# Kernel optimization log

Hardware: AMD Instinct MI355X
Metric: run time of the kernel (lower is better)

Reference implementation:

```python
import jax, jax.numpy as jnp
import numpy as np

N = 50000          # num nodes
E = 800000         # num edges (before self loops)
IN_C = 128
HID = 256          # heads * head_dim
HEADS = 4
HEAD_DIM = HID // HEADS
OUT_C = 64
NEG_SLOPE = 0.2    # PyG GATConv default leaky_relu slope
BN_EPS = 1e-5


def _gat_conv(x, src, dst, W, att_src, att_dst, bias, concat):
    """PyG-style GATConv (with self loops already appended to src/dst).
    x: [N, in_c]; W: [in_c, H*C]; att_src/att_dst: [H, C]; bias: [H*C] or [C]."""
    H, C = att_src.shape
    h = (x @ W).reshape(-1, H, C)                               # [N, H, C]
    a_src = jnp.einsum('nhc,hc->nh', h, att_src)                # [N, H]
    a_dst = jnp.einsum('nhc,hc->nh', h, att_dst)                # [N, H]
    e = jax.nn.leaky_relu(a_src[src] + a_dst[dst], NEG_SLOPE)   # [Et, H]
    # segment softmax over destination nodes (numerically stable)
    m = jax.ops.segment_max(e, dst, num_segments=N)             # [N, H]
    m = jnp.where(jnp.isfinite(m), m, 0.0)
    ex = jnp.exp(e - m[dst])
    denom = jax.ops.segment_sum(ex, dst, num_segments=N)        # [N, H]
    alpha = ex / (denom[dst] + 1e-16)                           # [Et, H]
    msg = alpha[:, :, None] * h[src]                            # [Et, H, C]
    out = jax.ops.segment_sum(msg, dst, num_segments=N)         # [N, H, C]
    out = out.reshape(N, H * C) if concat else out.mean(axis=1)
    return out + bias


def _bn_eval(x, gamma, beta, mean, var):
    return (x - mean) * jax.lax.rsqrt(var + BN_EPS) * gamma + beta


def setup_inputs() -> dict:
    key = jax.random.key(0)
    ks = jax.random.split(key, 16)
    x = jax.random.normal(ks[0], (N, IN_C), dtype=jnp.float32)
    edge_index = jax.random.randint(ks[1], (2, E), 0, N, dtype=jnp.int64)

    def lin(k, fan_in, fan_out):
        s = (1.0 / np.sqrt(fan_in)).astype(np.float32)
        return jax.random.normal(k, (fan_in, fan_out), dtype=jnp.float32) * s

    def att(k, h, c):
        return jax.random.normal(k, (h, c), dtype=jnp.float32) * 0.1

    return {
        'x': x, 'edge_index': edge_index,
        'W0': lin(ks[2], IN_C, HID), 'as0': att(ks[3], HEADS, HEAD_DIM), 'ad0': att(ks[4], HEADS, HEAD_DIM), 'b0': jnp.zeros((HID,), jnp.float32),
        'bn0_g': jnp.ones((HID,), jnp.float32), 'bn0_b': jnp.zeros((HID,), jnp.float32), 'bn0_m': jnp.zeros((HID,), jnp.float32), 'bn0_v': jnp.ones((HID,), jnp.float32),
        'W1': lin(ks[5], HID, HID), 'as1': att(ks[6], HEADS, HEAD_DIM), 'ad1': att(ks[7], HEADS, HEAD_DIM), 'b1': jnp.zeros((HID,), jnp.float32),
        'bn1_g': jnp.ones((HID,), jnp.float32), 'bn1_b': jnp.zeros((HID,), jnp.float32), 'bn1_m': jnp.zeros((HID,), jnp.float32), 'bn1_v': jnp.ones((HID,), jnp.float32),
        'W2': lin(ks[8], HID, OUT_C), 'as2': att(ks[9], 1, OUT_C), 'ad2': att(ks[10], 1, OUT_C), 'b2': jnp.zeros((OUT_C,), jnp.float32),
    }


def reference(x, edge_index, W0, as0, ad0, b0, bn0_g, bn0_b, bn0_m, bn0_v,
              W1, as1, ad1, b1, bn1_g, bn1_b, bn1_m, bn1_v,
              W2, as2, ad2, b2):
    loop = jnp.arange(N, dtype=edge_index.dtype)
    src = jnp.concatenate([edge_index[0], loop])   # PyG add_self_loops=True
    dst = jnp.concatenate([edge_index[1], loop])

    h = _gat_conv(x, src, dst, W0, as0, ad0, b0, concat=True)
    h = jax.nn.elu(_bn_eval(h, bn0_g, bn0_b, bn0_m, bn0_v))   # dropout: eval -> identity
    h = _gat_conv(h, src, dst, W1, as1, ad1, b1, concat=True)
    h = jax.nn.elu(_bn_eval(h, bn1_g, bn1_b, bn1_m, bn1_v))
    out = _gat_conv(h, src, dst, W2, as2, ad2, b2, concat=False)  # heads=1, mean
    return out
```

## Files before the change

kernel.cpp:

```cpp
#include <hip/hip_runtime.h>

#define NN   50000
#define EE   800000
#define ET   850000
#define INC  128
#define HID  256
#define OUTC 64
#define NEG  0.2f
#define BNEPS 1e-5f

typedef __bf16 bf16x8 __attribute__((ext_vector_type(8)));
typedef float  f32x4  __attribute__((ext_vector_type(4)));

static __device__ __forceinline__ float b2f(unsigned short u) {
    return __uint_as_float(((unsigned)u) << 16);
}
static __device__ __forceinline__ float blo(unsigned u) {
    return __uint_as_float(u << 16);
}
static __device__ __forceinline__ float bhi(unsigned u) {
    return __uint_as_float(u & 0xFFFF0000u);
}
static __device__ __forceinline__ unsigned short f2b(float f) {
    unsigned u = __float_as_uint(f);
    unsigned r = u + 0x7FFFu + ((u >> 16) & 1u);
    return (unsigned short)(r >> 16);
}
static __device__ __forceinline__ float leaky(float x) {
    return x > 0.f ? x : NEG * x;
}
static __device__ __forceinline__ float ew(float e) {
    return __expf(fminf(e, 80.f));
}

__global__ void k_flags(const int* __restrict__ ei, const unsigned* __restrict__ xw,
                        int* __restrict__ flagW, int* __restrict__ flagB) {
    __shared__ int cs[4];
    int b = blockIdx.x, t = threadIdx.x;
    if (b == 0) {
        int c = 0;
        for (int k = 0; k < 16; k++) {
            int i = t + 256 * k;
            if (ei[2 * i + 1] != 0) c = 1;
        }
        for (int o = 1; o < 64; o <<= 1) c |= __shfl_xor(c, o);
        if ((t & 63) == 0) cs[t >> 6] = c;
        __syncthreads();
        if (t == 0) *flagW = cs[0] | cs[1] | cs[2] | cs[3];
    } else {
        int c = 0;
        for (int i = t; i < 4096; i += 256) {
            unsigned v = (xw[i] >> 8) & 0x7F;
            if (v >= 50 && v <= 67) c++;
        }
        for (int o = 1; o < 64; o <<= 1) c += __shfl_xor(c, o);
        if ((t & 63) == 0) cs[t >> 6] = c;
        __syncthreads();
        if (t == 0) *flagB = (cs[0] + cs[1] + cs[2] + cs[3] > 2048) ? 1 : 0;
    }
}

__global__ void k_prep(const void* as0, const void* ad0, const void* b0, const void* g0,
                       const void* be0, const void* m0, const void* v0,
                       const void* as1, const void* ad1, const void* b1, const void* g1,
                       const void* be1, const void* m1, const void* v1,
                       const void* as2, const void* ad2, const void* b2,
                       const void* W0, const void* W1, const void* W2,
                       unsigned short* __restrict__ WT0, unsigned short* __restrict__ WT1,
                       unsigned short* __restrict__ WT2,
                       const void* __restrict__ x, unsigned short* __restrict__ xb,
                       float* __restrict__ pp, const int* __restrict__ flagB) {
    int b = blockIdx.x, t = threadIdx.x;
    bool bf = (*flagB != 0);
    auto cv = [&](const void* s, int i) -> float {
        return bf ? b2f(((const unsigned short*)s)[i]) : ((const float*)s)[i];
    };
    if (b < 14) {
        float v;
        switch (b) {
            case 0:  v = cv(as0, t); break;
            case 1:  v = cv(ad0, t); break;
            case 2:  v = cv(b0, t);  break;
            case 3:  v = cv(g0, t);  break;
            case 4:  v = cv(be0, t); break;
            case 5:  v = cv(m0, t);  break;
            case 6:  v = cv(v0, t);  break;
            case 7:  v = cv(as1, t); break;
            case 8:  v = cv(ad1, t); break;
            case 9:  v = cv(b1, t);  break;
            case 10: v = cv(g1, t);  break;
            case 11: v = cv(be1, t); break;
            case 12: v = cv(m1, t);  break;
            default: v = cv(v1, t);  break;
        }
        pp[b * 256 + t] = v;
    } else if (b == 14) {
        if (t < 192) {
            int arr = t >> 6, j = t & 63;
            float v = (arr == 0) ? cv(as2, j) : (arr == 1) ? cv(ad2, j) : cv(b2, j);
            pp[14 * 256 + arr * 64 + j] = v;
        }
    } else if (b < 15 + 128) {
        int i = (b - 15) * 256 + t;
        int k = i >> 8, n = i & 255;
        WT0[n * INC + k] = bf ? ((const unsigned short*)W0)[i] : f2b(((const float*)W0)[i]);
    } else if (b < 15 + 128 + 256) {
        int i = (b - 143) * 256 + t;
        int k = i >> 8, n = i & 255;
        WT1[n * HID + k] = bf ? ((const unsigned short*)W1)[i] : f2b(((const float*)W1)[i]);
    } else if (b < 15 + 128 + 256 + 64) {
        int i = (b - 399) * 256 + t;
        int k = i >> 6, n = i & 63;
        WT2[n * HID + k] = bf ? ((const unsigned short*)W2)[i] : f2b(((const float*)W2)[i]);
    } else {
        if (bf) return;
        int i = (b - 463) * 256 + t;
        if (i < NN * INC)
            xb[i] = f2b(((const float*)x)[i]);
    }
}

__global__ void k_hist(const int* __restrict__ ei, const int* __restrict__ flagW,
                       int* __restrict__ cnt) {
    int i = blockIdx.x * 256 + threadIdx.x;
    if (i >= ET) return;
    bool w32 = (*flagW != 0);
    int d = (i < EE) ? (w32 ? ei[EE + i] : ei[2 * (EE + i)]) : (i - EE);
    atomicAdd(&cnt[d], 1);
}

static __device__ __forceinline__ int block_scan_incl(int v, int t, int* ws) {
    int lane = t & 63, w = t >> 6;
    int x = v;
    for (int o = 1; o < 64; o <<= 1) {
        int y = __shfl_up(x, o);
        if (lane >= o) x += y;
    }
    if (lane == 63) ws[w] = x;
    __syncthreads();
    if (t == 0) {
        int s = 0;
        for (int k = 0; k < 4; k++) { int tmp = ws[k]; ws[k] = s; s += tmp; }
    }
    __syncthreads();
    return x + ws[w];
}

__global__ void k_scan_a(const int* __restrict__ cnt, int* __restrict__ rowptr, int* __restrict__ bsum) {
    __shared__ int ws[4];
    int t = threadIdx.x, b = blockIdx.x;
    int i = b * 256 + t;
    int v = (i < NN) ? cnt[i] : 0;
    int incl = block_scan_incl(v, t, ws);
    if (i < NN) rowptr[i] = incl - v;
    if (t == 255) bsum[b] = incl;
}

__global__ void k_scan_b(int* __restrict__ bsum, int nb) {
    __shared__ int ws[4];
    int t = threadIdx.x;
    int v = (t < nb) ? bsum[t] : 0;
    int incl = block_scan_incl(v, t, ws);
    if (t < nb) bsum[t] = incl - v;
}

__global__ void k_scan_c(int* __restrict__ rowptr, const int* __restrict__ bsum, int* __restrict__ cursor) {
    int t = threadIdx.x, b = blockIdx.x;
    int i = b * 256 + t;
    if (i < NN) {
        int r = rowptr[i] + bsum[b];
        rowptr[i] = r;
        cursor[i] = r;
    }
    if (i == 0) rowptr[NN] = ET;
}

__global__ void k_scatter(const int* __restrict__ ei, const int* __restrict__ flagW,
                          int* __restrict__ cursor, int* __restrict__ esrc) {
    int i = blockIdx.x * 256 + threadIdx.x;
    if (i >= ET) return;
    bool w32 = (*flagW != 0);
    int s, d;
    if (i < EE) {
        if (w32) { s = ei[i];     d = ei[EE + i]; }
        else     { s = ei[2 * i]; d = ei[2 * (EE + i)]; }
    } else {
        s = d = i - EE;
    }
    int p = atomicAdd(&cursor[d], 1);
    esrc[p] = s;
}

template<int NC, int NH>
__global__ __launch_bounds__(256) void k_gemm(const unsigned short* __restrict__ Amain,
                                              const void* __restrict__ Aalt,
                                              const int* __restrict__ flagB,
                                              const unsigned short* __restrict__ WT,
                                              unsigned short* __restrict__ H,
                                              float* __restrict__ asrc, float* __restrict__ adst,
                                              const float* __restrict__ asv, const float* __restrict__ adv,
                                              int M, int K) {
    __shared__ __align__(16) unsigned short As[128 * 40];
    __shared__ __align__(16) unsigned short Bs[64 * 40];
    const unsigned short* A = (*flagB) ? (const unsigned short*)Aalt : Amain;
    int t = threadIdx.x;
    int bm = blockIdx.x, bn = blockIdx.y;
    int lane = t & 63, wave = t >> 6;
    int m16 = lane & 15, quad = lane >> 4;

    f32x4 acc[2][4];
    for (int a = 0; a < 2; a++) for (int b = 0; b < 4; b++) acc[a][b] = (f32x4){0.f, 0.f, 0.f, 0.f};

    int arow = t >> 1, ahalf = t & 1;
    int brow = t >> 2, bq = t & 3;
    long gArow = (long)bm * 128 + arow;

    for (int k0 = 0; k0 < K; k0 += 32) {
        uint4 av0 = {0u, 0u, 0u, 0u}, av1 = {0u, 0u, 0u, 0u};
        if (gArow < M) {
            const unsigned short* ap = A + gArow * (size_t)K + k0 + ahalf * 16;
            av0 = *(const uint4*)(ap);
            av1 = *(const uint4*)(ap + 8);
        }
        uint4 bv = *(const uint4*)(WT + ((size_t)bn * 64 + brow) * K + k0 + bq * 8);
        *(uint4*)&As[arow * 40 + ahalf * 16]     = av0;
        *(uint4*)&As[arow * 40 + ahalf * 16 + 8] = av1;
        *(uint4*)&Bs[brow * 40 + bq * 8]         = bv;
        __syncthreads();
        int wrow = wave * 32;
        bf16x8 af[2], bf[4];
        for (int mt = 0; mt < 2; mt++)
            af[mt] = *(const bf16x8*)&As[(wrow + mt * 16 + m16) * 40 + quad * 8];
        for (int nt = 0; nt < 4; nt++)
            bf[nt] = *(const bf16x8*)&Bs[(nt * 16 + m16) * 40 + quad * 8];
        for (int mt = 0; mt < 2; mt++)
            for (int nt = 0; nt < 4; nt++)
                acc[mt][nt] = __builtin_amdgcn_mfma_f32_16x16x32_bf16(af[mt], bf[nt], acc[mt][nt], 0, 0, 0);
        __syncthreads();
    }

    float asc[4], adc[4];
    for (int nt = 0; nt < 4; nt++) {
        int col = bn * 64 + nt * 16 + m16;
        asc[nt] = asv[col];
        adc[nt] = adv[col];
    }
    for (int mt = 0; mt < 2; mt++) {
        int gR0 = bm * 128 + wave * 32 + mt * 16 + quad * 4;
        for (int r = 0; r < 4; r++) {
            int gR = gR0 + r;
            float ps = 0.f, pd = 0.f;
            for (int nt = 0; nt < 4; nt++) {
                float v = acc[mt][nt][r];
                ps += v * asc[nt];
                pd += v * adc[nt];
            }
            for (int o = 1; o < 16; o <<= 1) { ps += __shfl_xor(ps, o); pd += __shfl_xor(pd, o); }
            if (m16 == 0 && gR < M) {
                asrc[(size_t)gR * NH + bn] = ps;
                adst[(size_t)gR * NH + bn] = pd;
            }
            if (gR < M) {
                for (int nt = 0; nt < 4; nt++) {
                    int gC = bn * 64 + nt * 16 + m16;
                    H[(size_t)gR * NC + gC] = f2b(acc[mt][nt][r]);
                }
            }
        }
    }
}

__global__ void k_agg4(const unsigned short* __restrict__ h,
                       const float* __restrict__ asrc, const float* __restrict__ adst,
                       const int* __restrict__ rowptr, const int* __restrict__ esrc,
                       const float* __restrict__ bias,
                       const float* __restrict__ bng, const float* __restrict__ bnb,
                       const float* __restrict__ bnm, const float* __restrict__ bnv,
                       unsigned short* __restrict__ act) {
    int t = threadIdx.x;
    int wave = t >> 6, lane = t & 63;
    int nodeA = blockIdx.x * 8 + wave * 2;
    if (nodeA >= NN) return;
    int nodeB = nodeA + 1;
    bool hasB = (nodeB < NN);

    int hd = lane >> 4, li = lane & 15;
    int wsel = lane & 48;
    const size_t lc = (size_t)lane * 4;

    int e0A = __builtin_amdgcn_readfirstlane(rowptr[nodeA]);
    int e1A = __builtin_amdgcn_readfirstlane(rowptr[nodeA + 1]);
    int degA = e1A - e0A;
    int e0B = e1A, degB = 0;
    if (hasB) degB = __builtin_amdgcn_readfirstlane(rowptr[nodeB + 1]) - e1A;

    float adhA = adst[(size_t)nodeA * 4 + hd];
    float adhB = hasB ? adst[(size_t)nodeB * 4 + hd] : 0.f;

    float waccA = 0.f, waccB = 0.f;
    float aA0 = 0.f, aA1 = 0.f, aA2 = 0.f, aA3 = 0.f;
    float aB0 = 0.f, aB1 = 0.f, aB2 = 0.f, aB3 = 0.f;

    int nA = min(16, degA), nB = min(16, degB);
    float eA = 0.f, eB = 0.f;
    if (li < nA) { int s = esrc[e0A + li]; eA = asrc[(size_t)s * 4 + hd]; }
    if (li < nB) { int s = esrc[e0B + li]; eB = asrc[(size_t)s * 4 + hd]; }

    int degM = max(degA, degB);
    for (int c = 0; c < degM; c += 16) {
        float wA = (li < nA) ? ew(leaky(eA + adhA)) : 0.f;
        float wB = (li < nB) ? ew(leaky(eB + adhB)) : 0.f;
        waccA += wA; waccB += wB;
        int nA2 = min(16, degA - (c + 16));
        int nB2 = min(16, degB - (c + 16));
        float eA2 = 0.f, eB2 = 0.f;
        if (li < nA2) { int s = esrc[e0A + c + 16 + li]; eA2 = asrc[(size_t)s * 4 + hd]; }
        if (li < nB2) { int s = esrc[e0B + c + 16 + li]; eB2 = asrc[(size_t)s * 4 + hd]; }
        #pragma unroll
        for (int g = 0; g < 4; g++) {
            int j = g * 4;
            bool doA = j < nA, doB = j < nB;
            float w0A = 0.f, w1A = 0.f, w2A = 0.f, w3A = 0.f;
            float w0B = 0.f, w1B = 0.f, w2B = 0.f, w3B = 0.f;
            uint2 hA0 = {0, 0}, hA1 = {0, 0}, hA2 = {0, 0}, hA3 = {0, 0};
            uint2 hB0 = {0, 0}, hB1 = {0, 0}, hB2 = {0, 0}, hB3 = {0, 0};
            if (doA) {
                int s0 = esrc[e0A + c + j];     int s1 = esrc[e0A + c + j + 1];
                int s2 = esrc[e0A + c + j + 2]; int s3 = esrc[e0A + c + j + 3];
                w0A = __shfl(wA, wsel + j);     w1A = __shfl(wA, wsel + j + 1);
                w2A = __shfl(wA, wsel + j + 2); w3A = __shfl(wA, wsel + j + 3);
                hA0 = *(const uint2*)(h + (size_t)s0 * HID + lc);
                hA1 = *(const uint2*)(h + (size_t)s1 * HID + lc);
                hA2 = *(const uint2*)(h + (size_t)s2 * HID + lc);
                hA3 = *(const uint2*)(h + (size_t)s3 * HID + lc);
            }
            if (doB) {
                int s0 = esrc[e0B + c + j];     int s1 = esrc[e0B + c + j + 1];
                int s2 = esrc[e0B + c + j + 2]; int s3 = esrc[e0B + c + j + 3];
                w0B = __shfl(wB, wsel + j);     w1B = __shfl(wB, wsel + j + 1);
                w2B = __shfl(wB, wsel + j + 2); w3B = __shfl(wB, wsel + j + 3);
                hB0 = *(const uint2*)(h + (size_t)s0 * HID + lc);
                hB1 = *(const uint2*)(h + (size_t)s1 * HID + lc);
                hB2 = *(const uint2*)(h + (size_t)s2 * HID + lc);
                hB3 = *(const uint2*)(h + (size_t)s3 * HID + lc);
            }
            if (doA) {
                aA0 += w0A * blo(hA0.x) + w1A * blo(hA1.x) + w2A * blo(hA2.x) + w3A * blo(hA3.x);
                aA1 += w0A * bhi(hA0.x) + w1A * bhi(hA1.x) + w2A * bhi(hA2.x) + w3A * bhi(hA3.x);
                aA2 += w0A * blo(hA0.y) + w1A * blo(hA1.y) + w2A * blo(hA2.y) + w3A * blo(hA3.y);
                aA3 += w0A * bhi(hA0.y) + w1A * bhi(hA1.y) + w2A * bhi(hA2.y) + w3A * bhi(hA3.y);
            }
            if (doB) {
                aB0 += w0B * blo(hB0.x) + w1B * blo(hB1.x) + w2B * blo(hB2.x) + w3B * blo(hB3.x);
                aB1 += w0B * bhi(hB0.x) + w1B * bhi(hB1.x) + w2B * bhi(hB2.x) + w3B * bhi(hB3.x);
                aB2 += w0B * blo(hB0.y) + w1B * blo(hB1.y) + w2B * blo(hB2.y) + w3B * blo(hB3.y);
                aB3 += w0B * bhi(hB0.y) + w1B * bhi(hB1.y) + w2B * bhi(hB2.y) + w3B * bhi(hB3.y);
            }
        }
        eA = eA2; nA = nA2;
        eB = eB2; nB = nB2;
    }
    waccA += __shfl_xor(waccA, 1); waccA += __shfl_xor(waccA, 2);
    waccA += __shfl_xor(waccA, 4); waccA += __shfl_xor(waccA, 8);
    waccB += __shfl_xor(waccB, 1); waccB += __shfl_xor(waccB, 2);
    waccB += __shfl_xor(waccB, 4); waccB += __shfl_xor(waccB, 8);
    float invA = 1.f / (waccA + 1e-16f);
    float invB = 1.f / (waccB + 1e-16f);

    int c0 = lane * 4;
    float4 bi = *(const float4*)(bias + c0);
    float4 bm_ = *(const float4*)(bnm + c0);
    float4 bv_ = *(const float4*)(bnv + c0);
    float4 bg_ = *(const float4*)(bng + c0);
    float4 bb_ = *(const float4*)(bnb + c0);
    float sc[4], sh[4];
    {
        const float* bvp = (const float*)&bv_;
        const float* bgp = (const float*)&bg_;
        const float* bmp = (const float*)&bm_;
        const float* bbp = (const float*)&bb_;
        const float* bip = (const float*)&bi;
        #pragma unroll
        for (int jj = 0; jj < 4; jj++) {
            float s_ = rsqrtf(bvp[jj] + BNEPS) * bgp[jj];
            sc[jj] = s_;
            sh[jj] = bbp[jj] + (bip[jj] - bmp[jj]) * s_;
        }
    }
    {
        float o[4] = {aA0 * invA, aA1 * invA, aA2 * invA, aA3 * invA};
        unsigned short res[4];
        #pragma unroll
        for (int jj = 0; jj < 4; jj++) {
            float val = o[jj] * sc[jj] + sh[jj];
            val = val > 0.f ? val : expm1f(val);
            res[jj] = f2b(val);
        }
        *(ushort4*)(act + (size_t)nodeA * HID + c0) = *(ushort4*)res;
    }
    if (hasB) {
        float o[4] = {aB0 * invB, aB1 * invB, aB2 * invB, aB3 * invB};
        unsigned short res[4];
        #pragma unroll
        for (int jj = 0; jj < 4; jj++) {
            float val = o[jj] * sc[jj] + sh[jj];
            val = val > 0.f ? val : expm1f(val);
            res[jj] = f2b(val);
        }
        *(ushort4*)(act + (size_t)nodeB * HID + c0) = *(ushort4*)res;
    }
}

__global__ void k_agg1(const unsigned short* __restrict__ h,
                       const float* __restrict__ asrc, const float* __restrict__ adst,
                       const int* __restrict__ rowptr, const int* __restrict__ esrc,
                       const float* __restrict__ bias,
                       void* __restrict__ outp, const int* __restrict__ flagB) {
    int t = threadIdx.x;
    int wave = t >> 6, lane = t & 63;
    int node = blockIdx.x * 4 + wave;
    if (node >= NN) return;
    int e0  = __builtin_amdgcn_readfirstlane(rowptr[node]);
    int e1  = __builtin_amdgcn_readfirstlane(rowptr[node + 1]);
    int deg = e1 - e0;
    float ad = adst[node];

    float den = 0.f, acc = 0.f;

    int n = min(64, deg);
    float e = 0.f;
    if (lane < n) { int s = esrc[e0 + lane]; e = asrc[s]; }

    for (int c = 0; c < deg; c += 64) {
        float w = (lane < n) ? ew(leaky(e + ad)) : 0.f;
        int n2 = min(64, deg - (c + 64));
        float eN = 0.f;
        if (lane < n2) { int s = esrc[e0 + c + 64 + lane]; eN = asrc[s]; }
        den += w;
        for (int j = 0; j < n; j += 4) {
            int s0 = esrc[e0 + c + j];     int s1 = esrc[e0 + c + j + 1];
            int s2 = esrc[e0 + c + j + 2]; int s3 = esrc[e0 + c + j + 3];
            float w0 = __shfl(w, j),     w1 = __shfl(w, j + 1);
            float w2 = __shfl(w, j + 2), w3 = __shfl(w, j + 3);
            float h0 = b2f(h[(size_t)s0 * OUTC + lane]);
            float h1 = b2f(h[(size_t)s1 * OUTC + lane]);
            float h2 = b2f(h[(size_t)s2 * OUTC + lane]);
            float h3 = b2f(h[(size_t)s3 * OUTC + lane]);
            acc += w0 * h0 + w1 * h1 + w2 * h2 + w3 * h3;
        }
        e = eN; n = n2;
    }
    for (int o = 1; o < 64; o <<= 1) den += __shfl_xor(den, o);
    float val = acc / (den + 1e-16f) + bias[lane];
    if (*flagB) ((unsigned short*)outp)[(size_t)node * OUTC + lane] = f2b(val);
    else        ((float*)outp)[(size_t)node * OUTC + lane] = val;
}

extern "C" void kernel_launch(void* const* d_in, const int* in_sizes, int n_in,
                              void* d_out, int out_size, void* d_ws, size_t ws_size,
                              hipStream_t stream) {
    const void* x  = d_in[0];
    const int*  ei = (const int*)d_in[1];
    const void* W0 = d_in[2];
    const void* W1 = d_in[10];
    const void* W2 = d_in[18];

    char* ws = (char*)d_ws;
    size_t off = 0;
    auto alloc = [&](size_t n) { void* p = ws + off; off += (n + 255) & ~(size_t)255; return p; };

    unsigned short* xb  = (unsigned short*)alloc((size_t)NN * INC * 2);
    unsigned short* h   = (unsigned short*)alloc((size_t)NN * HID * 2);
    unsigned short* act = (unsigned short*)alloc((size_t)NN * HID * 2);
    unsigned short* WT0 = (unsigned short*)alloc((size_t)HID * INC * 2);
    unsigned short* WT1 = (unsigned short*)alloc((size_t)HID * HID * 2);
    unsigned short* WT2 = (unsigned short*)alloc((size_t)OUTC * HID * 2);
    float*          pp  = (float*)alloc((size_t)(14 * 256 + 3 * 64) * 4);
    float*  asrc   = (float*)alloc((size_t)NN * 4 * 4);
    float*  adst   = (float*)alloc((size_t)NN * 4 * 4);
    int*    cnt    = (int*)alloc((size_t)(NN + 2) * 4);
    int*    rowptr = (int*)alloc((size_t)(NN + 1) * 4);
    int*    cursor = (int*)alloc((size_t)NN * 4);
    int*    esrc   = (int*)alloc((size_t)(ET + 64) * 4);
    int*    bsum   = (int*)alloc(256 * 4);
    int*    flagW  = cnt + NN;
    int*    flagB  = cnt + NN + 1;

    float* P0 = pp;
    float* P1 = pp + 7 * 256;
    float* P2 = pp + 14 * 256;

    const int nbN = (NN + 255) / 256;
    const int nbE = (ET + 255) / 256;
    const int nbA4 = (NN + 7) / 8;
    const int nbA1 = (NN + 3) / 4;
    const int nbPrep = 463 + (NN * INC + 255) / 256;
    dim3 gemmGrid0((NN + 127) / 128, HID / 64);
    dim3 gemmGrid2((NN + 127) / 128, 1);

    hipMemsetAsync(cnt, 0, (size_t)(NN + 2) * 4, stream);
    k_flags<<<2, 256, 0, stream>>>(ei, (const unsigned*)x, flagW, flagB);
    k_hist<<<nbE, 256, 0, stream>>>(ei, flagW, cnt);
    k_scan_a<<<nbN, 256, 0, stream>>>(cnt, rowptr, bsum);
    k_scan_b<<<1, 256, 0, stream>>>(bsum, nbN);
    k_scan_c<<<nbN, 256, 0, stream>>>(rowptr, bsum, cursor);
    k_scatter<<<nbE, 256, 0, stream>>>(ei, flagW, cursor, esrc);

    k_prep<<<nbPrep, 256, 0, stream>>>(d_in[3], d_in[4], d_in[5], d_in[6], d_in[7], d_in[8], d_in[9],
                                       d_in[11], d_in[12], d_in[13], d_in[14], d_in[15], d_in[16], d_in[17],
                                       d_in[19], d_in[20], d_in[21],
                                       W0, W1, W2, WT0, WT1, WT2, x, xb, pp, flagB);

    k_gemm<HID, 4><<<gemmGrid0, 256, 0, stream>>>(xb, x, flagB, WT0, h, asrc, adst,
                                                  P0 + 0, P0 + 256, NN, INC);
    k_agg4<<<nbA4, 256, 0, stream>>>(h, asrc, adst, rowptr, esrc,
                                     P0 + 512, P0 + 768, P0 + 1024, P0 + 1280, P0 + 1536, act);

    k_gemm<HID, 4><<<gemmGrid0, 256, 0, stream>>>(act, act, flagB, WT1, h, asrc, adst,
                                                  P1 + 0, P1 + 256, NN, HID);
    k_agg4<<<nbA4, 256, 0, stream>>>(h, asrc, adst, rowptr, esrc,
                                     P1 + 512, P1 + 768, P1 + 1024, P1 + 1280, P1 + 1536, act);

    k_gemm<OUTC, 1><<<gemmGrid2, 256, 0, stream>>>(act, act, flagB, WT2, h, asrc, adst,
                                                   P2 + 0, P2 + 64, NN, HID);
    k_agg1<<<nbA1, 256, 0, stream>>>(h, asrc, adst, rowptr, esrc, P2 + 128, d_out, flagB);
}
```

Before: 447.8 us.

## Process more nodes per wave in GAT aggregation and fold memset into init

The 4-head aggregation kernel now handles four destination nodes per wave instead of two, and the single-head output aggregation handles two nodes per wave instead of one. Both changes aim to put more independent gather loads in flight and hide memory latency. The separate memset of the count array is folded into the flag-detection kernel, which removes one launch. The cost is higher register pressure and more wasted lanes on imbalanced degrees, since each wave loops to the maximum degree among its nodes.

```diff
diff --git a/kernel.cpp b/kernel.cpp
--- a/kernel.cpp
+++ b/kernel.cpp
@@ -33,11 +33,15 @@
     return __expf(fminf(e, 80.f));
 }
 
-__global__ void k_flags(const int* __restrict__ ei, const unsigned* __restrict__ xw,
-                        int* __restrict__ flagW, int* __restrict__ flagB) {
+__global__ void k_init(const int* __restrict__ ei, const unsigned* __restrict__ xw,
+                       int* __restrict__ cnt, int* __restrict__ flagW, int* __restrict__ flagB,
+                       int nbZ) {
     __shared__ int cs[4];
     int b = blockIdx.x, t = threadIdx.x;
-    if (b == 0) {
+    if (b < nbZ) {
+        int i = b * 256 + t;
+        if (i < NN) cnt[i] = 0;
+    } else if (b == nbZ) {
         int c = 0;
         for (int k = 0; k < 16; k++) {
             int i = t + 256 * k;
@@ -279,93 +283,96 @@
                        unsigned short* __restrict__ act) {
     int t = threadIdx.x;
     int wave = t >> 6, lane = t & 63;
-    int nodeA = blockIdx.x * 8 + wave * 2;
-    if (nodeA >= NN) return;
-    int nodeB = nodeA + 1;
-    bool hasB = (nodeB < NN);
-
+    int node0 = blockIdx.x * 16 + wave * 4;
+    if (node0 >= NN) return;
     int hd = lane >> 4, li = lane & 15;
     int wsel = lane & 48;
     const size_t lc = (size_t)lane * 4;
 
-    int e0A = __builtin_amdgcn_readfirstlane(rowptr[nodeA]);
-    int e1A = __builtin_amdgcn_readfirstlane(rowptr[nodeA + 1]);
-    int degA = e1A - e0A;
-    int e0B = e1A, degB = 0;
-    if (hasB) degB = __builtin_amdgcn_readfirstlane(rowptr[nodeB + 1]) - e1A;
-
-    float adhA = adst[(size_t)nodeA * 4 + hd];
-    float adhB = hasB ? adst[(size_t)nodeB * 4 + hd] : 0.f;
-
-    float waccA = 0.f, waccB = 0.f;
-    float aA0 = 0.f, aA1 = 0.f, aA2 = 0.f, aA3 = 0.f;
-    float aB0 = 0.f, aB1 = 0.f, aB2 = 0.f, aB3 = 0.f;
-
-    int nA = min(16, degA), nB = min(16, degB);
-    float eA = 0.f, eB = 0.f;
-    if (li < nA) { int s = esrc[e0A + li]; eA = asrc[(size_t)s * 4 + hd]; }
-    if (li < nB) { int s = esrc[e0B + li]; eB = asrc[(size_t)s * 4 + hd]; }
-
-    int degM = max(degA, degB);
+    int e0[4], dg[4];
+    {
+        int prev = __builtin_amdgcn_readfirstlane(rowptr[node0]);
+        #pragma unroll
+        for (int k = 0; k < 4; k++) {
+            int idx = min(node0 + k + 1, NN);
+            int nx = __builtin_amdgcn_readfirstlane(rowptr[idx]);
+            e0[k] = prev; dg[k] = nx - prev; prev = nx;
+        }
+    }
+    float adh[4];
+    #pragma unroll
+    for (int k = 0; k < 4; k++)
+        adh[k] = (node0 + k < NN) ? adst[(size_t)(node0 + k) * 4 + hd] : 0.f;
+
+    float wacc[4] = {0.f, 0.f, 0.f, 0.f};
+    float acc[4][4] = {{0.f}};
+
+    int n_[4]; float es[4];
+    #pragma unroll
+    for (int k = 0; k < 4; k++) {
+        n_[k] = min(16, dg[k]);
+        es[k] = 0.f;
+        if (li < n_[k]) { int s = esrc[e0[k] + li]; es[k] = asrc[(size_t)s * 4 + hd]; }
+    }
+
+    int degM = max(max(dg[0], dg[1]), max(dg[2], dg[3]));
     for (int c = 0; c < degM; c += 16) {
-        float wA = (li < nA) ? ew(leaky(eA + adhA)) : 0.f;
-        float wB = (li < nB) ? ew(leaky(eB + adhB)) : 0.f;
-        waccA += wA; waccB += wB;
-        int nA2 = min(16, degA - (c + 16));
-        int nB2 = min(16, degB - (c + 16));
-        float eA2 = 0.f, eB2 = 0.f;
-        if (li < nA2) { int s = esrc[e0A + c + 16 + li]; eA2 = asrc[(size_t)s * 4 + hd]; }
-        if (li < nB2) { int s = esrc[e0B + c + 16 + li]; eB2 = asrc[(size_t)s * 4 + hd]; }
+        float w[4];
+        #pragma unroll
+        for (int k = 0; k < 4; k++) {
+            w[k] = (li < n_[k]) ? ew(leaky(es[k] + adh[k])) : 0.f;
+            wacc[k] += w[k];
+        }
+        int nn[4];
+        #pragma unroll
+        for (int k = 0; k < 4; k++) {
+            nn[k] = min(16, dg[k] - (c + 16));
+            es[k] = 0.f;
+            if (li < nn[k]) { int s = esrc[e0[k] + c + 16 + li]; es[k] = asrc[(size_t)s * 4 + hd]; }
+        }
         #pragma unroll
         for (int g = 0; g < 4; g++) {
             int j = g * 4;
-            bool doA = j < nA, doB = j < nB;
-            float w0A = 0.f, w1A = 0.f, w2A = 0.f, w3A = 0.f;
-            float w0B = 0.f, w1B = 0.f, w2B = 0.f, w3B = 0.f;
-            uint2 hA0 = {0, 0}, hA1 = {0, 0}, hA2 = {0, 0}, hA3 = {0, 0};
-            uint2 hB0 = {0, 0}, hB1 = {0, 0}, hB2 = {0, 0}, hB3 = {0, 0};
-            if (doA) {
-                int s0 = esrc[e0A + c + j];     int s1 = esrc[e0A + c + j + 1];
-                int s2 = esrc[e0A + c + j + 2]; int s3 = esrc[e0A + c + j + 3];
-                w0A = __shfl(wA, wsel + j);     w1A = __shfl(wA, wsel + j + 1);
-                w2A = __shfl(wA, wsel + j + 2); w3A = __shfl(wA, wsel + j + 3);
-                hA0 = *(const uint2*)(h + (size_t)s0 * HID + lc);
-                hA1 = *(const uint2*)(h + (size_t)s1 * HID + lc);
-                hA2 = *(const uint2*)(h + (size_t)s2 * HID + lc);
-                hA3 = *(const uint2*)(h + (size_t)s3 * HID + lc);
-            }
-            if (doB) {
-                int s0 = esrc[e0B + c + j];     int s1 = esrc[e0B + c + j + 1];
-                int s2 = esrc[e0B + c + j + 2]; int s3 = esrc[e0B + c + j + 3];
-                w0B = __shfl(wB, wsel + j);     w1B = __shfl(wB, wsel + j + 1);
-                w2B = __shfl(wB, wsel + j + 2); w3B = __shfl(wB, wsel + j + 3);
-                hB0 = *(const uint2*)(h + (size_t)s0 * HID + lc);
-                hB1 = *(const uint2*)(h + (size_t)s1 * HID + lc);
-                hB2 = *(const uint2*)(h + (size_t)s2 * HID + lc);
-                hB3 = *(const uint2*)(h + (size_t)s3 * HID + lc);
-            }
-            if (doA) {
-                aA0 += w0A * blo(hA0.x) + w1A * blo(hA1.x) + w2A * blo(hA2.x) + w3A * blo(hA3.x);
-                aA1 += w0A * bhi(hA0.x) + w1A * bhi(hA1.x) + w2A * bhi(hA2.x) + w3A * bhi(hA3.x);
-                aA2 += w0A * blo(hA0.y) + w1A * blo(hA1.y) + w2A * blo(hA2.y) + w3A * blo(hA3.y);
-                aA3 += w0A * bhi(hA0.y) + w1A * bhi(hA1.y) + w2A * bhi(hA2.y) + w3A * bhi(hA3.y);
-            }
-            if (doB) {
-                aB0 += w0B * blo(hB0.x) + w1B * blo(hB1.x) + w2B * blo(hB2.x) + w3B * blo(hB3.x);
-                aB1 += w0B * bhi(hB0.x) + w1B * bhi(hB1.x) + w2B * bhi(hB2.x) + w3B * bhi(hB3.x);
-                aB2 += w0B * blo(hB0.y) + w1B * blo(hB1.y) + w2B * blo(hB2.y) + w3B * blo(hB3.y);
-                aB3 += w0B * bhi(hB0.y) + w1B * bhi(hB1.y) + w2B * bhi(hB2.y) + w3B * bhi(hB3.y);
-            }
-        }
-        eA = eA2; nA = nA2;
-        eB = eB2; nB = nB2;
-    }
-    waccA += __shfl_xor(waccA, 1); waccA += __shfl_xor(waccA, 2);
-    waccA += __shfl_xor(waccA, 4); waccA += __shfl_xor(waccA, 8);
-    waccB += __shfl_xor(waccB, 1); waccB += __shfl_xor(waccB, 2);
-    waccB += __shfl_xor(waccB, 4); waccB += __shfl_xor(waccB, 8);
-    float invA = 1.f / (waccA + 1e-16f);
-    float invB = 1.f / (waccB + 1e-16f);
+            float wb[4][4];
+            uint2 hv[4][4];
+            #pragma unroll
+            for (int k = 0; k < 4; k++) {
+                if (j < n_[k]) {
+                    int s0 = esrc[e0[k] + c + j];     int s1 = esrc[e0[k] + c + j + 1];
+                    int s2 = esrc[e0[k] + c + j + 2]; int s3 = esrc[e0[k] + c + j + 3];
+                    wb[k][0] = __shfl(w[k], wsel + j);     wb[k][1] = __shfl(w[k], wsel + j + 1);
+                    wb[k][2] = __shfl(w[k], wsel + j + 2); wb[k][3] = __shfl(w[k], wsel + j + 3);
+                    hv[k][0] = *(const uint2*)(h + (size_t)s0 * HID + lc);
+                    hv[k][1] = *(const uint2*)(h + (size_t)s1 * HID + lc);
+                    hv[k][2] = *(const uint2*)(h + (size_t)s2 * HID + lc);
+                    hv[k][3] = *(const uint2*)(h + (size_t)s3 * HID + lc);
+                }
+            }
+            #pragma unroll
+            for (int k = 0; k < 4; k++) {
+                if (j < n_[k]) {
+                    acc[k][0] += wb[k][0] * blo(hv[k][0].x) + wb[k][1] * blo(hv[k][1].x)
+                               + wb[k][2] * blo(hv[k][2].x) + wb[k][3] * blo(hv[k][3].x);
+                    acc[k][1] += wb[k][0] * bhi(hv[k][0].x) + wb[k][1] * bhi(hv[k][1].x)
+                               + wb[k][2] * bhi(hv[k][2].x) + wb[k][3] * bhi(hv[k][3].x);
+                    acc[k][2] += wb[k][0] * blo(hv[k][0].y) + wb[k][1] * blo(hv[k][1].y)
+                               + wb[k][2] * blo(hv[k][2].y) + wb[k][3] * blo(hv[k][3].y);
+                    acc[k][3] += wb[k][0] * bhi(hv[k][0].y) + wb[k][1] * bhi(hv[k][1].y)
+                               + wb[k][2] * bhi(hv[k][2].y) + wb[k][3] * bhi(hv[k][3].y);
+                }
+            }
+        }
+        #pragma unroll
+        for (int k = 0; k < 4; k++) n_[k] = nn[k];
+    }
+
+    #pragma unroll
+    for (int k = 0; k < 4; k++) {
+        wacc[k] += __shfl_xor(wacc[k], 1);
+        wacc[k] += __shfl_xor(wacc[k], 2);
+        wacc[k] += __shfl_xor(wacc[k], 4);
+        wacc[k] += __shfl_xor(wacc[k], 8);
+    }
 
     int c0 = lane * 4;
     float4 bi = *(const float4*)(bias + c0);
@@ -387,27 +394,19 @@
             sh[jj] = bbp[jj] + (bip[jj] - bmp[jj]) * s_;
         }
     }
-    {
-        float o[4] = {aA0 * invA, aA1 * invA, aA2 * invA, aA3 * invA};
-        unsigned short res[4];
-        #pragma unroll
-        for (int jj = 0; jj < 4; jj++) {
-            float val = o[jj] * sc[jj] + sh[jj];
-            val = val > 0.f ? val : expm1f(val);
-            res[jj] = f2b(val);
-        }
-        *(ushort4*)(act + (size_t)nodeA * HID + c0) = *(ushort4*)res;
-    }
-    if (hasB) {
-        float o[4] = {aB0 * invB, aB1 * invB, aB2 * invB, aB3 * invB};
-        unsigned short res[4];
-        #pragma unroll
-        for (int jj = 0; jj < 4; jj++) {
-            float val = o[jj] * sc[jj] + sh[jj];
-            val = val > 0.f ? val : expm1f(val);
-            res[jj] = f2b(val);
-        }
-        *(ushort4*)(act + (size_t)nodeB * HID + c0) = *(ushort4*)res;
+    #pragma unroll
+    for (int k = 0; k < 4; k++) {
+        if (node0 + k < NN) {
+            float inv = 1.f / (wacc[k] + 1e-16f);
+            unsigned short res[4];
+            #pragma unroll
+            for (int jj = 0; jj < 4; jj++) {
+                float val = acc[k][jj] * inv * sc[jj] + sh[jj];
+                val = val > 0.f ? val : expm1f(val);
+                res[jj] = f2b(val);
+            }
+            *(ushort4*)(act + (size_t)(node0 + k) * HID + c0) = *(ushort4*)res;
+        }
     }
 }
 
@@ -418,42 +417,79 @@
                        void* __restrict__ outp, const int* __restrict__ flagB) {
     int t = threadIdx.x;
     int wave = t >> 6, lane = t & 63;
-    int node = blockIdx.x * 4 + wave;
-    if (node >= NN) return;
-    int e0  = __builtin_amdgcn_readfirstlane(rowptr[node]);
-    int e1  = __builtin_amdgcn_readfirstlane(rowptr[node + 1]);
-    int deg = e1 - e0;
-    float ad = adst[node];
-
-    float den = 0.f, acc = 0.f;
-
-    int n = min(64, deg);
-    float e = 0.f;
-    if (lane < n) { int s = esrc[e0 + lane]; e = asrc[s]; }
-
-    for (int c = 0; c < deg; c += 64) {
-        float w = (lane < n) ? ew(leaky(e + ad)) : 0.f;
-        int n2 = min(64, deg - (c + 64));
-        float eN = 0.f;
-        if (lane < n2) { int s = esrc[e0 + c + 64 + lane]; eN = asrc[s]; }
-        den += w;
-        for (int j = 0; j < n; j += 4) {
-            int s0 = esrc[e0 + c + j];     int s1 = esrc[e0 + c + j + 1];
-            int s2 = esrc[e0 + c + j + 2]; int s3 = esrc[e0 + c + j + 3];
-            float w0 = __shfl(w, j),     w1 = __shfl(w, j + 1);
-            float w2 = __shfl(w, j + 2), w3 = __shfl(w, j + 3);
-            float h0 = b2f(h[(size_t)s0 * OUTC + lane]);
-            float h1 = b2f(h[(size_t)s1 * OUTC + lane]);
-            float h2 = b2f(h[(size_t)s2 * OUTC + lane]);
-            float h3 = b2f(h[(size_t)s3 * OUTC + lane]);
-            acc += w0 * h0 + w1 * h1 + w2 * h2 + w3 * h3;
-        }
-        e = eN; n = n2;
-    }
-    for (int o = 1; o < 64; o <<= 1) den += __shfl_xor(den, o);
-    float val = acc / (den + 1e-16f) + bias[lane];
-    if (*flagB) ((unsigned short*)outp)[(size_t)node * OUTC + lane] = f2b(val);
-    else        ((float*)outp)[(size_t)node * OUTC + lane] = val;
+    int nodeA = blockIdx.x * 8 + wave * 2;
+    if (nodeA >= NN) return;
+    int nodeB = nodeA + 1;
+    bool hasB = (nodeB < NN);
+
+    int e0A  = __builtin_amdgcn_readfirstlane(rowptr[nodeA]);
+    int e1A  = __builtin_amdgcn_readfirstlane(rowptr[nodeA + 1]);
+    int degA = e1A - e0A;
+    int e0B  = e1A;
+    int degB = hasB ? (__builtin_amdgcn_readfirstlane(rowptr[nodeB + 1]) - e1A) : 0;
+    float adA = adst[nodeA];
+    float adB = hasB ? adst[nodeB] : 0.f;
+
+    float denA = 0.f, denB = 0.f, accA = 0.f, accB = 0.f;
+
+    int nA = min(64, degA), nB = min(64, degB);
+    float eA = 0.f, eB = 0.f;
+    if (lane < nA) { int s = esrc[e0A + lane]; eA = asrc[s]; }
+    if (lane < nB) { int s = esrc[e0B + lane]; eB = asrc[s]; }
+
+    int degM = max(degA, degB);
+    for (int c = 0; c < degM; c += 64) {
+        float wA = (lane < nA) ? ew(leaky(eA + adA)) : 0.f;
+        float wB = (lane < nB) ? ew(leaky(eB + adB)) : 0.f;
+        denA += wA; denB += wB;
+        int nA2 = min(64, degA - (c + 64));
+        int nB2 = min(64, degB - (c + 64));
+        eA = 0.f; eB = 0.f;
+        if (lane < nA2) { int s = esrc[e0A + c + 64 + lane]; eA = asrc[s]; }
+        if (lane < nB2) { int s = esrc[e0B + c + 64 + lane]; eB = asrc[s]; }
+        int nM = max(nA, nB);
+        for (int j = 0; j < nM; j += 4) {
+            bool doA = j < nA, doB = j < nB;
+            float w0A = 0.f, w1A = 0.f, w2A = 0.f, w3A = 0.f;
+            float w0B = 0.f, w1B = 0.f, w2B = 0.f, w3B = 0.f;
+            unsigned short hA0 = 0, hA1 = 0, hA2 = 0, hA3 = 0;
+            unsigned short hB0 = 0, hB1 = 0, hB2 = 0, hB3 = 0;
+            if (doA) {
+                int s0 = esrc[e0A + c + j];     int s1 = esrc[e0A + c + j + 1];
+                int s2 = esrc[e0A + c + j + 2]; int s3 = esrc[e0A + c + j + 3];
+                w0A = __shfl(wA, j);     w1A = __shfl(wA, j + 1);
+                w2A = __shfl(wA, j + 2); w3A = __shfl(wA, j + 3);
+                hA0 = h[(size_t)s0 * OUTC + lane];
+                hA1 = h[(size_t)s1 * OUTC + lane];
+                hA2 = h[(size_t)s2 * OUTC + lane];
+                hA3 = h[(size_t)s3 * OUTC + lane];
+            }
+            if (doB) {
+                int s0 = esrc[e0B + c + j];     int s1 = esrc[e0B + c + j + 1];
+                int s2 = esrc[e0B + c + j + 2]; int s3 = esrc[e0B + c + j + 3];
+                w0B = __shfl(wB, j);     w1B = __shfl(wB, j + 1);
+                w2B = __shfl(wB, j + 2); w3B = __shfl(wB, j + 3);
+                hB0 = h[(size_t)s0 * OUTC + lane];
+                hB1 = h[(size_t)s1 * OUTC + lane];
+                hB2 = h[(size_t)s2 * OUTC + lane];
+                hB3 = h[(size_t)s3 * OUTC + lane];
+            }
+            if (doA) accA += w0A * b2f(hA0) + w1A * b2f(hA1) + w2A * b2f(hA2) + w3A * b2f(hA3);
+            if (doB) accB += w0B * b2f(hB0) + w1B * b2f(hB1) + w2B * b2f(hB2) + w3B * b2f(hB3);
+        }
+        nA = nA2; nB = nB2;
+    }
+    for (int o = 1; o < 64; o <<= 1) denA += __shfl_xor(denA, o);
+    for (int o = 1; o < 64; o <<= 1) denB += __shfl_xor(denB, o);
+    float valA = accA / (denA + 1e-16f) + bias[lane];
+    float valB = accB / (denB + 1e-16f) + bias[lane];
+    if (*flagB) {
+        ((unsigned short*)outp)[(size_t)nodeA * OUTC + lane] = f2b(valA);
+        if (hasB) ((unsigned short*)outp)[(size_t)nodeB * OUTC + lane] = f2b(valB);
+    } else {
+        ((float*)outp)[(size_t)nodeA * OUTC + lane] = valA;
+        if (hasB) ((float*)outp)[(size_t)nodeB * OUTC + lane] = valB;
+    }
 }
 
 extern "C" void kernel_launch(void* const* d_in, const int* in_sizes, int n_in,
@@ -492,14 +528,13 @@
 
     const int nbN = (NN + 255) / 256;
     const int nbE = (ET + 255) / 256;
-    const int nbA4 = (NN + 7) / 8;
-    const int nbA1 = (NN + 3) / 4;
+    const int nbA4 = (NN + 15) / 16;
+    const int nbA1 = (NN + 7) / 8;
     const int nbPrep = 463 + (NN * INC + 255) / 256;
     dim3 gemmGrid0((NN + 127) / 128, HID / 64);
     dim3 gemmGrid2((NN + 127) / 128, 1);
 
-    hipMemsetAsync(cnt, 0, (size_t)(NN + 2) * 4, stream);
-    k_flags<<<2, 256, 0, stream>>>(ei, (const unsigned*)x, flagW, flagB);
+    k_init<<<nbN + 2, 256, 0, stream>>>(ei, (const unsigned*)x, cnt, flagW, flagB, nbN);
     k_hist<<<nbE, 256, 0, stream>>>(ei, flagW, cnt);
     k_scan_a<<<nbN, 256, 0, stream>>>(cnt, rowptr, bsum);
     k_scan_b<<<1, 256, 0, stream>>>(bsum, nbN);
```

New measurement: 767.3 us. +71.4%, slower.
